# Kernel tuning notes

Measured on AMD Instinct MI355X. Metric: run time of the kernel, lower is better.

The kernel has to match this reference:

```python
import jax, jax.numpy as jnp
import numpy as np

EPS = 1e-8

def setup_inputs() -> dict:
    key = jax.random.key(0)
    k1, k2 = jax.random.split(key)
    B, IN, OUT, G = 32768, 256, 256, 5
    x = jax.random.normal(k1, (B, IN), dtype=jnp.float32)
    grid = jnp.linspace(-1.0, 1.0, G).astype(jnp.float32)
    coef = jax.random.normal(k2, (OUT, IN, G), dtype=jnp.float32) * 0.1
    scale = jnp.ones((OUT, IN), dtype=jnp.float32)
    bias = jnp.zeros((OUT,), dtype=jnp.float32)
    return {"x": x, "grid": grid, "coef": coef, "scale": scale, "bias": bias}

def reference(x, grid, coef, scale, bias):
    # global min-max normalization to [-1, 1]
    xmin, xmax = x.min(), x.max()
    xn = 2.0 * (x - xmin) / (xmax - xmin + EPS) - 1.0
    # cubic bump B-spline-like basis: (batch, in, grid)
    dist = jnp.abs(xn[..., None] - grid)
    basis = jnp.where(dist < 1.0, 1.0 - dist ** 3, 0.0)
    basis = basis / (basis.sum(axis=-1, keepdims=True) + EPS)
    # fused contraction over (in, grid); equals ((basis*coef).sum(-1)*scale).sum(-1)
    w = coef * scale[..., None]          # (out, in, grid)
    out = jnp.einsum('big,oig->bo', basis, w) + bias
    return out
```

## Files before the change

kernel.cpp:

```cpp
#include <hip/hip_runtime.h>
#include <stdint.h>


#define B_SZ   32768
#define IN_SZ  256
#define OUT_SZ 256
#define EPSF   1e-8f

typedef __bf16 bf16x8 __attribute__((ext_vector_type(8)));
typedef unsigned short ushort8 __attribute__((ext_vector_type(8)));
typedef float floatx16 __attribute__((ext_vector_type(16)));

union frag_u { uint4 u; bf16x8 v; };

__device__ __forceinline__ unsigned short f2bf(float f) {
  unsigned u = __float_as_uint(f);
  u += 0x7FFFu + ((u >> 16) & 1u);
  return (unsigned short)(u >> 16);
}


__global__ void __launch_bounds__(256) prep_kernel(const float* __restrict__ coef,
                                                   const float* __restrict__ scale,
                                                   const float* __restrict__ x,
                                                   unsigned short* __restrict__ wf,
                                                   float* __restrict__ part, int n4) {
  const int t = threadIdx.x;
  if (blockIdx.x < 256) {
    int idx = blockIdx.x * 256 + t;
    int o = idx >> 8, i = idx & 255;
    float s = scale[idx];
    const float* c = coef + (size_t)idx * 5;
    ushort8 v;
    v[0] = f2bf(c[0] * s); v[1] = f2bf(c[1] * s); v[2] = f2bf(c[2] * s);
    v[3] = f2bf(c[3] * s); v[4] = f2bf(c[4] * s);
    v[5] = 0; v[6] = 0; v[7] = 0;
    int chunk = (((o >> 5) * 64 + (i >> 2)) * 2 + ((i >> 1) & 1)) * 64
                + (i & 1) * 32 + (o & 31);
    *(ushort8*)(wf + (size_t)chunk * 8) = v;
  } else {
    int mb = blockIdx.x - 256;
    const float4* x4 = (const float4*)x;
    float lmin = 1e30f, lmax = -1e30f;
    for (int i = mb * 256 + t; i < n4; i += 256 * 256) {
      float4 v = x4[i];
      lmin = fminf(lmin, fminf(fminf(v.x, v.y), fminf(v.z, v.w)));
      lmax = fmaxf(lmax, fmaxf(fmaxf(v.x, v.y), fmaxf(v.z, v.w)));
    }
    #pragma unroll
    for (int off = 32; off >= 1; off >>= 1) {
      lmin = fminf(lmin, __shfl_down(lmin, off, 64));
      lmax = fmaxf(lmax, __shfl_down(lmax, off, 64));
    }
    __shared__ float smn[4], smx[4];
    if ((t & 63) == 0) { smn[t >> 6] = lmin; smx[t >> 6] = lmax; }
    __syncthreads();
    if (t == 0) {
      part[2 * mb]     = fminf(fminf(smn[0], smn[1]), fminf(smn[2], smn[3]));
      part[2 * mb + 1] = fmaxf(fmaxf(smx[0], smx[1]), fmaxf(smx[2], smx[3]));
    }
  }
}

__device__ __forceinline__ bf16x8 basisfrag(float xval, float scA, float scB) {
  float xn = fmaf(xval, scA, scB);
  float d0 = xn + 1.0f, d1 = xn + 0.5f, d3 = xn - 0.5f, d4 = xn - 1.0f;
  float b0 = fmaxf(fmaf(d0 * d0, -fabsf(d0), 1.0f), 0.0f);
  float b1 = fmaxf(fmaf(d1 * d1, -fabsf(d1), 1.0f), 0.0f);
  float b2 = fmaxf(fmaf(xn * xn, -fabsf(xn), 1.0f), 0.0f);
  float b3 = fmaxf(fmaf(d3 * d3, -fabsf(d3), 1.0f), 0.0f);
  float b4 = fmaxf(fmaf(d4 * d4, -fabsf(d4), 1.0f), 0.0f);
  float sum = ((b0 + b1) + (b2 + b3)) + b4;
  float inv = __builtin_amdgcn_rcpf(sum);
  b0 *= inv; b1 *= inv; b2 *= inv; b3 *= inv; b4 *= inv;
  frag_u r;
  r.u.x = __builtin_amdgcn_perm(__float_as_uint(b1), __float_as_uint(b0), 0x07060302u);
  r.u.y = __builtin_amdgcn_perm(__float_as_uint(b3), __float_as_uint(b2), 0x07060302u);
  r.u.z = __float_as_uint(b4) >> 16;
  r.u.w = 0u;
  return r.v;
}

__global__ void __launch_bounds__(256, 2) kan_gemm(
    const float* __restrict__ x,
    const unsigned short* __restrict__ wf,
    const float* __restrict__ bias,
    const float* __restrict__ part,
    float* __restrict__ out)
{
  __shared__ __align__(16) unsigned short Bb[2][16384];
  __shared__ float2 red[4];

  const int t = threadIdx.x;
  const int lane = t & 63;
  const int wm = t >> 6;
  const int l31 = lane & 31, lh = lane >> 5;
  const int bRow = blockIdx.x * 128;
  const int bCol = blockIdx.y * 128;
  const int row = bRow + wm * 32 + l31;

  auto stage = [&](int c, int buf) {
    #pragma unroll
    for (int r = 0; r < 8; ++r) {
      int idx = r * 4 + wm;
      const unsigned short* src = wf +
          ((size_t)(((blockIdx.y * 4 + (idx >> 3)) * 64 + (c * 4 + ((idx >> 1) & 3))) * 2
                    + (idx & 1))) * 512 + (size_t)lane * 8;
      __builtin_amdgcn_global_load_lds(
          (const __attribute__((address_space(1))) unsigned int*)src,
          (__attribute__((address_space(3))) unsigned int*)(&Bb[buf][idx * 512 + lane * 8]),
          16, 0, 0);
    }
  };

  const float* xrow = x + (size_t)row * IN_SZ;

  stage(0, 0);
  float4 xq[4], xqn[4];
  #pragma unroll
  for (int g = 0; g < 4; ++g) xq[g] = *(const float4*)(xrow + g * 4);

  float2 p = ((const float2*)part)[t];
  float mn = p.x, mx = p.y;
  #pragma unroll
  for (int off = 32; off >= 1; off >>= 1) {
    mn = fminf(mn, __shfl_down(mn, off, 64));
    mx = fmaxf(mx, __shfl_down(mx, off, 64));
  }
  if (lane == 0) red[wm] = make_float2(mn, mx);
  __syncthreads();
  mn = fminf(fminf(red[0].x, red[1].x), fminf(red[2].x, red[3].x));
  mx = fmaxf(fmaxf(red[0].y, red[1].y), fmaxf(red[2].y, red[3].y));
  const float scA = 2.0f / (mx - mn + EPSF);
  const float scB = -mn * scA - 1.0f;

  floatx16 acc[4] = {};
  bf16x8 br[2][8];

  auto ldsB = [&](int ktr, int buf, bf16x8* dst) {
    #pragma unroll
    for (int q = 0; q < 8; ++q) {
      int ni = q >> 1, ks = q & 1;
      dst[q] = *(const bf16x8*)(&Bb[buf][((ni * 4 + ktr) * 2 + ks) * 512 + lane * 8]);
    }
  };

  for (int c = 0; c < 16; ++c) {
    const int buf = c & 1;

    __syncthreads();

    if (c < 15) {
      stage(c + 1, buf ^ 1);
      #pragma unroll
      for (int g = 0; g < 4; ++g)
        xqn[g] = *(const float4*)(xrow + (c + 1) * 16 + g * 4);
    }

    ldsB(0, buf, br[0]);

    #pragma unroll
    for (int ktr = 0; ktr < 4; ++ktr) {
      if (ktr < 3) ldsB(ktr + 1, buf, br[(ktr + 1) & 1]);

      float xv0 = lh ? xq[ktr].y : xq[ktr].x;
      float xv1 = lh ? xq[ktr].w : xq[ktr].z;
      bf16x8 af0 = basisfrag(xv0, scA, scB);
      bf16x8 af1 = basisfrag(xv1, scA, scB);

      bf16x8* B = br[ktr & 1];
      #pragma unroll
      for (int ni = 0; ni < 4; ++ni)
        acc[ni] = __builtin_amdgcn_mfma_f32_32x32x16_bf16(af0, B[ni * 2 + 0], acc[ni], 0, 0, 0);
      #pragma unroll
      for (int ni = 0; ni < 4; ++ni)
        acc[ni] = __builtin_amdgcn_mfma_f32_32x32x16_bf16(af1, B[ni * 2 + 1], acc[ni], 0, 0, 0);
    }

    if (c < 15) {
      #pragma unroll
      for (int g = 0; g < 4; ++g) xq[g] = xqn[g];
    }
  }

  #pragma unroll
  for (int ni = 0; ni < 4; ++ni) {
    int o = bCol + ni * 32 + l31;
    float bs = bias[o];
    int rb = bRow + wm * 32 + 4 * lh;
    #pragma unroll
    for (int reg = 0; reg < 16; ++reg) {
      int r = rb + (reg & 3) + 8 * (reg >> 2);
      out[(size_t)r * OUT_SZ + o] = acc[ni][reg] + bs;
    }
  }
}

extern "C" void kernel_launch(void* const* d_in, const int* in_sizes, int n_in,
                              void* d_out, int out_size, void* d_ws, size_t ws_size,
                              hipStream_t stream) {
  const float* x     = (const float*)d_in[0];
  const float* coef  = (const float*)d_in[2];
  const float* scale = (const float*)d_in[3];
  const float* bias  = (const float*)d_in[4];
  float* out = (float*)d_out;

  size_t need = 4096 + (size_t)OUT_SZ * IN_SZ * 8 * 2;
  if (ws_size < need) return;

  float* part = (float*)d_ws;
  unsigned short* wf = (unsigned short*)((char*)d_ws + 4096);

  prep_kernel<<<512, 256, 0, stream>>>(coef, scale, x, wf, part,
                                       (B_SZ * IN_SZ) / 4);
  dim3 g(B_SZ / 128, OUT_SZ / 128);
  kan_gemm<<<g, 256, 0, stream>>>(x, wf, bias, part, out);
}
```

Before: 135.0 us.

## Widen min/max reduction grid, pair column tiles, hoist basis computation

The min/max reduction now runs on 2048 blocks, each doing a fixed 4 float4 loads instead of a strided loop, to expose more memory parallelism. The GEMM kernel keeps the two output column tiles of a row block adjacent in a 1D grid so both tiles can reuse x in cache. The basis fragments for all four k-steps are computed before the MFMA loop, which separates VALU work from matrix instructions but keeps more registers live. The gemm prologue now reduces 2048 partials per block instead of 256.

Result: no change. 132.4 us (-1.9%).

```diff
diff --git a/kernel.cpp b/kernel.cpp
--- a/kernel.cpp
+++ b/kernel.cpp
@@ -6,6 +6,7 @@
 #define IN_SZ  256
 #define OUT_SZ 256
 #define EPSF   1e-8f
+#define NMB    2048
 
 typedef __bf16 bf16x8 __attribute__((ext_vector_type(8)));
 typedef unsigned short ushort8 __attribute__((ext_vector_type(8)));
@@ -41,9 +42,11 @@
   } else {
     int mb = blockIdx.x - 256;
     const float4* x4 = (const float4*)x;
+    int i = mb * 256 + t;
     float lmin = 1e30f, lmax = -1e30f;
-    for (int i = mb * 256 + t; i < n4; i += 256 * 256) {
-      float4 v = x4[i];
+    #pragma unroll
+    for (int k = 0; k < 4; ++k) {
+      float4 v = x4[i + k * (NMB * 256)];
       lmin = fminf(lmin, fminf(fminf(v.x, v.y), fminf(v.z, v.w)));
       lmax = fmaxf(lmax, fmaxf(fmaxf(v.x, v.y), fmaxf(v.z, v.w)));
     }
@@ -95,8 +98,10 @@
   const int lane = t & 63;
   const int wm = t >> 6;
   const int l31 = lane & 31, lh = lane >> 5;
-  const int bRow = blockIdx.x * 128;
-  const int bCol = blockIdx.y * 128;
+  const int by = blockIdx.x & 1;
+  const int bx = blockIdx.x >> 1;
+  const int bRow = bx * 128;
+  const int bCol = by * 128;
   const int row = bRow + wm * 32 + l31;
 
   auto stage = [&](int c, int buf) {
@@ -104,7 +109,7 @@
     for (int r = 0; r < 8; ++r) {
       int idx = r * 4 + wm;
       const unsigned short* src = wf +
-          ((size_t)(((blockIdx.y * 4 + (idx >> 3)) * 64 + (c * 4 + ((idx >> 1) & 3))) * 2
+          ((size_t)(((by * 4 + (idx >> 3)) * 64 + (c * 4 + ((idx >> 1) & 3))) * 2
                     + (idx & 1))) * 512 + (size_t)lane * 8;
       __builtin_amdgcn_global_load_lds(
           (const __attribute__((address_space(1))) unsigned int*)src,
@@ -120,8 +125,13 @@
   #pragma unroll
   for (int g = 0; g < 4; ++g) xq[g] = *(const float4*)(xrow + g * 4);
 
-  float2 p = ((const float2*)part)[t];
-  float mn = p.x, mx = p.y;
+  float mn = 1e30f, mx = -1e30f;
+  const float2* part2 = (const float2*)part;
+  #pragma unroll
+  for (int k = 0; k < NMB / 256; ++k) {
+    float2 p = part2[k * 256 + t];
+    mn = fminf(mn, p.x); mx = fmaxf(mx, p.y);
+  }
   #pragma unroll
   for (int off = 32; off >= 1; off >>= 1) {
     mn = fminf(mn, __shfl_down(mn, off, 64));
@@ -159,22 +169,23 @@
 
     ldsB(0, buf, br[0]);
 
+    bf16x8 af0[4], af1[4];
+    #pragma unroll
+    for (int ktr = 0; ktr < 4; ++ktr) {
+      af0[ktr] = basisfrag(lh ? xq[ktr].y : xq[ktr].x, scA, scB);
+      af1[ktr] = basisfrag(lh ? xq[ktr].w : xq[ktr].z, scA, scB);
+    }
+
     #pragma unroll
     for (int ktr = 0; ktr < 4; ++ktr) {
       if (ktr < 3) ldsB(ktr + 1, buf, br[(ktr + 1) & 1]);
-
-      float xv0 = lh ? xq[ktr].y : xq[ktr].x;
-      float xv1 = lh ? xq[ktr].w : xq[ktr].z;
-      bf16x8 af0 = basisfrag(xv0, scA, scB);
-      bf16x8 af1 = basisfrag(xv1, scA, scB);
-
       bf16x8* B = br[ktr & 1];
       #pragma unroll
       for (int ni = 0; ni < 4; ++ni)
-        acc[ni] = __builtin_amdgcn_mfma_f32_32x32x16_bf16(af0, B[ni * 2 + 0], acc[ni], 0, 0, 0);
+        acc[ni] = __builtin_amdgcn_mfma_f32_32x32x16_bf16(af0[ktr], B[ni * 2 + 0], acc[ni], 0, 0, 0);
       #pragma unroll
       for (int ni = 0; ni < 4; ++ni)
-        acc[ni] = __builtin_amdgcn_mfma_f32_32x32x16_bf16(af1, B[ni * 2 + 1], acc[ni], 0, 0, 0);
+        acc[ni] = __builtin_amdgcn_mfma_f32_32x32x16_bf16(af1[ktr], B[ni * 2 + 1], acc[ni], 0, 0, 0);
     }
 
     if (c < 15) {
@@ -205,14 +216,13 @@
   const float* bias  = (const float*)d_in[4];
   float* out = (float*)d_out;
 
-  size_t need = 4096 + (size_t)OUT_SZ * IN_SZ * 8 * 2;
+  size_t need = 16384 + (size_t)OUT_SZ * IN_SZ * 8 * 2;
   if (ws_size < need) return;
 
   float* part = (float*)d_ws;
-  unsigned short* wf = (unsigned short*)((char*)d_ws + 4096);
-
-  prep_kernel<<<512, 256, 0, stream>>>(coef, scale, x, wf, part,
-                                       (B_SZ * IN_SZ) / 4);
-  dim3 g(B_SZ / 128, OUT_SZ / 128);
-  kan_gemm<<<g, 256, 0, stream>>>(x, wf, bias, part, out);
-}
+  unsigned short* wf = (unsigned short*)((char*)d_ws + 16384);
+
+  prep_kernel<<<256 + NMB, 256, 0, stream>>>(coef, scale, x, wf, part,
+                                             (B_SZ * IN_SZ) / 4);
+  kan_gemm<<<512, 256, 0, stream>>>(x, wf, bias, part, out);
+}
```
